# Kernel optimization log

Measured on AMD Instinct MI355X. Metric: run time of the kernel, lower is better.

Reference implementation:

```python
import jax, jax.numpy as jnp
import numpy as np
from jax import lax

B, T, D_IN, D_OUT = 8, 4096, 256, 256


def setup_inputs() -> dict:
    key = jax.random.key(0)
    k1, k2, k3, k4, k5 = jax.random.split(key, 5)
    bound_in = 1.0 / np.sqrt(D_IN)
    return {
        "inputs": jax.random.normal(k1, (B, T, D_IN), dtype=jnp.float32),
        "mask": jnp.zeros((B, T, 1), dtype=jnp.float32),
        "W_in": jax.random.uniform(k2, (D_OUT, D_IN), jnp.float32, -bound_in, bound_in),
        "b_in": jax.random.uniform(k3, (D_OUT,), jnp.float32, -bound_in, bound_in),
        "W_f": jax.random.uniform(k4, (D_OUT, D_IN), jnp.float32, -bound_in, bound_in),
        "b_f": jax.random.uniform(k5, (D_OUT,), jnp.float32, -bound_in, bound_in),
    }


def _forget_mult(f, x):
    # h_t = f_t * x_t + (1 - f_t) * h_{t-1}, h_{-1} = 0 (torchqrnn ForgetMult, hidden_init=None)
    fT = jnp.swapaxes(f, 0, 1)  # (T, B, D)
    xT = jnp.swapaxes(x, 0, 1)

    def step(h, fx):
        ft, xt = fx
        h = ft * xt + (1.0 - ft) * h
        return h, h

    h0 = jnp.zeros(xT.shape[1:], dtype=x.dtype)  # (B, D)
    _, hs = lax.scan(step, h0, (fT, xT))
    return jnp.swapaxes(hs, 0, 1)  # (B, T, D)


def reference(inputs, mask, W_in, b_in, W_f, b_f):
    # right_to_left = False -> no flips
    x = jnp.tanh(jnp.einsum("btd,od->bto", inputs, W_in) + b_in)
    f = jax.nn.sigmoid(jnp.einsum("btd,od->bto", inputs, W_f) + b_f + mask * 10000.0)
    return _forget_mult(f, x)
```

## Files before the change

### kernel.cpp

```cpp
#include <hip/hip_runtime.h>
#include <math.h>


typedef _Float16 f16x8 __attribute__((ext_vector_type(8)));
typedef _Float16 f16x4_t __attribute__((ext_vector_type(4)));
typedef float f32x4 __attribute__((ext_vector_type(4)));

constexpr int B_ = 8, T_ = 4096, D_ = 256, K_ = 256;
constexpr int M_ = B_ * T_;
constexpr int CHUNK = 64;
constexpr int NCH = T_ / CHUNK;

struct alignas(4) XF { _Float16 x, f; };

__device__ __forceinline__ float fexp2(float a) { return __builtin_amdgcn_exp2f(a); }
__device__ __forceinline__ float frcp(float a) { return __builtin_amdgcn_rcpf(a); }
constexpr float L2E = 1.4426950408889634f;

__device__ __forceinline__ float fast_sigmoid(float z) {
  return frcp(1.f + fexp2(-z * L2E));
}
__device__ __forceinline__ float fast_tanh(float z) {
  const float t = fexp2(-2.f * L2E * fabsf(z));
  const float r = (1.f - t) * frcp(1.f + t);
  return copysignf(r, z);
}

__global__ __launch_bounds__(256) void wconv(const float* __restrict__ Win,
                                             const float* __restrict__ Wf,
                                             _Float16* __restrict__ Wh) {
  int i = (blockIdx.x * 256 + threadIdx.x) * 4;
  const float* src = (i < 65536) ? (Win + i) : (Wf + (i - 65536));
  f32x4 v = *(const f32x4*)src;
  f16x4_t o = { (_Float16)v[0], (_Float16)v[1], (_Float16)v[2], (_Float16)v[3] };
  *(f16x4_t*)(Wh + i) = o;
}

__global__ __launch_bounds__(256, 2) void gemm_act(
    const float* __restrict__ A, const _Float16* __restrict__ W,
    const float* __restrict__ bin, const float* __restrict__ bfv,
    const float* __restrict__ mask, XF* __restrict__ xf) {
  const int tid = threadIdx.x;
  const int w = tid >> 6, lane = tid & 63;
  const int quad = lane >> 4, l16 = lane & 15;
  const int mwb = (w >> 1) * 32, nwb = (w & 1) * 128;
  const int row0 = blockIdx.x * 64 + mwb;

  f32x4 acc[2][2][8];
#pragma unroll
  for (int a = 0; a < 2; ++a)
#pragma unroll
    for (int i = 0; i < 2; ++i)
#pragma unroll
      for (int j = 0; j < 8; ++j) acc[a][i][j] = (f32x4){0.f, 0.f, 0.f, 0.f};

  for (int kk = 0; kk < 8; ++kk) {
    const int k0 = kk * 32 + quad * 8;
    f16x8 afr[2];
#pragma unroll
    for (int mt = 0; mt < 2; ++mt) {
      const float* p = A + (size_t)(row0 + mt * 16 + l16) * K_ + k0;
      f32x4 lo = *(const f32x4*)p;
      f32x4 hi = *(const f32x4*)(p + 4);
      f16x8 t;
      t[0] = (_Float16)lo[0]; t[1] = (_Float16)lo[1];
      t[2] = (_Float16)lo[2]; t[3] = (_Float16)lo[3];
      t[4] = (_Float16)hi[0]; t[5] = (_Float16)hi[1];
      t[6] = (_Float16)hi[2]; t[7] = (_Float16)hi[3];
      afr[mt] = t;
    }
#pragma unroll
    for (int mat = 0; mat < 2; ++mat) {
      const _Float16* Wp = W + ((size_t)mat << 16);
      f16x8 bfr[8];
#pragma unroll
      for (int nt = 0; nt < 8; ++nt)
        bfr[nt] = *(const f16x8*)(Wp + (size_t)(nwb + nt * 16 + l16) * K_ + k0);
#pragma unroll
      for (int mt = 0; mt < 2; ++mt)
#pragma unroll
        for (int nt = 0; nt < 8; ++nt)
          acc[mat][mt][nt] = __builtin_amdgcn_mfma_f32_16x16x32_f16(
              afr[mt], bfr[nt], acc[mat][mt][nt], 0, 0, 0);
    }
  }

  float bx[8], bff[8];
#pragma unroll
  for (int nt = 0; nt < 8; ++nt) {
    const int col = nwb + nt * 16 + l16;
    bx[nt] = bin[col];
    bff[nt] = bfv[col];
  }
#pragma unroll
  for (int mt = 0; mt < 2; ++mt) {
#pragma unroll
    for (int r = 0; r < 4; ++r) {
      const int row = row0 + mt * 16 + quad * 4 + r;
      const float madd = 10000.f * mask[row];
#pragma unroll
      for (int nt = 0; nt < 8; ++nt) {
        const int col = nwb + nt * 16 + l16;
        const float zx = acc[0][mt][nt][r] + bx[nt];
        const float zf = acc[1][mt][nt][r] + bff[nt] + madd;
        XF v;
        v.x = (_Float16)fast_tanh(zx);
        v.f = (_Float16)fast_sigmoid(zf);
        xf[(size_t)row * D_ + col] = v;
      }
    }
  }
}

__global__ __launch_bounds__(256) void scan_a(const XF* __restrict__ xf,
                                              float* __restrict__ Ap,
                                              float* __restrict__ Hp) {
  const int d = threadIdx.x;
  const int g = blockIdx.x;
  const size_t base = (size_t)g * CHUNK * D_ + d;
  float Aacc = 1.f, h = 0.f;
#pragma unroll 8
  for (int i = 0; i < CHUNK; ++i) {
    const XF v = xf[base + (size_t)i * D_];
    const float f = (float)v.f;
    const float a = 1.f - f;
    h = f * (float)v.x + a * h;
    Aacc *= a;
  }
  Ap[(size_t)g * D_ + d] = Aacc;
  Hp[(size_t)g * D_ + d] = h;
}

__global__ __launch_bounds__(256) void scan_b(const float* __restrict__ Ap,
                                              const float* __restrict__ Hp,
                                              float* __restrict__ hs) {
  const int d = threadIdx.x, b = blockIdx.x;
  float h = 0.f;
#pragma unroll 8
  for (int c = 0; c < NCH; ++c) {
    const size_t idx = ((size_t)b * NCH + c) * D_ + d;
    hs[idx] = h;
    h = Hp[idx] + Ap[idx] * h;
  }
}

__global__ __launch_bounds__(256) void scan_c(const XF* __restrict__ xf,
                                              const float* __restrict__ hs,
                                              float* __restrict__ out) {
  const int d = threadIdx.x;
  const int g = blockIdx.x;
  float h = hs[(size_t)g * D_ + d];
  const size_t base = (size_t)g * CHUNK * D_ + d;
#pragma unroll 8
  for (int i = 0; i < CHUNK; ++i) {
    const XF v = xf[base + (size_t)i * D_];
    const float f = (float)v.f;
    h = f * (float)v.x + (1.f - f) * h;
    out[base + (size_t)i * D_] = h;
  }
}

extern "C" void kernel_launch(void* const* d_in, const int* in_sizes, int n_in,
                              void* d_out, int out_size, void* d_ws, size_t ws_size,
                              hipStream_t stream) {
  const float* inputs = (const float*)d_in[0];
  const float* mask   = (const float*)d_in[1];
  const float* W_in   = (const float*)d_in[2];
  const float* b_in   = (const float*)d_in[3];
  const float* W_f    = (const float*)d_in[4];
  const float* b_f    = (const float*)d_in[5];
  float* out = (float*)d_out;
  char* ws = (char*)d_ws;

  constexpr size_t XFSZ = (size_t)M_ * D_ * sizeof(XF);
  constexpr size_t WSZ  = (size_t)2 * 256 * 256 * 2;
  constexpr size_t SUM  = (size_t)B_ * NCH * D_ * sizeof(float);

  XF* xf = (XF*)ws;
  _Float16* Wh = (_Float16*)(ws + XFSZ);
  float* Ap = (float*)(ws + XFSZ + WSZ);
  float* Hp = Ap + SUM / sizeof(float);
  float* Hs = Hp + SUM / sizeof(float);

  wconv<<<128, 256, 0, stream>>>(W_in, W_f, Wh);
  gemm_act<<<512, 256, 0, stream>>>(inputs, Wh, b_in, b_f, mask, xf);
  scan_a<<<512, 256, 0, stream>>>(xf, Ap, Hp);
  scan_b<<<8, 256, 0, stream>>>(Ap, Hp, Hs);
  scan_c<<<512, 256, 0, stream>>>(xf, Hs, out);
}
```

Baseline: 151.6 us.

## Fuse chunk scan into LDS-staged GEMM and merge carry propagation into final scan

The GEMM now stages A and a pre-swizzled fp16 weight layout through LDS and uses 32x32x16 MFMA tiles. It writes the activated x/f tile to shared memory and runs the per-chunk scan in the same kernel, which drops the separate scan_a pass that re-read xf. scan_b is removed, and each final-scan block instead recomputes its own carry serially over the preceding chunk summaries. This cuts two launches and one full read of xf. The cost is 64KB of LDS per block, which limits occupancy, and a redundant carry loop of up to 63 steps per block.

```diff
diff --git a/kernel.cpp b/kernel.cpp
--- a/kernel.cpp
+++ b/kernel.cpp
@@ -3,8 +3,8 @@
 
 
 typedef _Float16 f16x8 __attribute__((ext_vector_type(8)));
-typedef _Float16 f16x4_t __attribute__((ext_vector_type(4)));
 typedef float f32x4 __attribute__((ext_vector_type(4)));
+typedef float f32x16 __attribute__((ext_vector_type(16)));
 
 constexpr int B_ = 8, T_ = 4096, D_ = 256, K_ = 256;
 constexpr int M_ = B_ * T_;
@@ -22,44 +22,57 @@
 }
 __device__ __forceinline__ float fast_tanh(float z) {
   const float t = fexp2(-2.f * L2E * fabsf(z));
-  const float r = (1.f - t) * frcp(1.f + t);
-  return copysignf(r, z);
+  return copysignf((1.f - t) * frcp(1.f + t), z);
 }
 
 __global__ __launch_bounds__(256) void wconv(const float* __restrict__ Win,
                                              const float* __restrict__ Wf,
-                                             _Float16* __restrict__ Wh) {
-  int i = (blockIdx.x * 256 + threadIdx.x) * 4;
-  const float* src = (i < 65536) ? (Win + i) : (Wf + (i - 65536));
-  f32x4 v = *(const f32x4*)src;
-  f16x4_t o = { (_Float16)v[0], (_Float16)v[1], (_Float16)v[2], (_Float16)v[3] };
-  *(f16x4_t*)(Wh + i) = o;
-}
-
-__global__ __launch_bounds__(256, 2) void gemm_act(
-    const float* __restrict__ A, const _Float16* __restrict__ W,
+                                             _Float16* __restrict__ Wh2) {
+  const int t = blockIdx.x * 256 + threadIdx.x;
+  const int n = t & 255;
+  const int kc = (t >> 8) & 3;
+  const int mat = (t >> 10) & 1;
+  const int kk = t >> 11;
+  const float* s = (mat ? Wf : Win) + (size_t)n * K_ + kk * 32 + kc * 8;
+  f32x4 a = *(const f32x4*)s;
+  f32x4 b = *(const f32x4*)(s + 4);
+  f16x8 o;
+  o[0] = (_Float16)a[0]; o[1] = (_Float16)a[1];
+  o[2] = (_Float16)a[2]; o[3] = (_Float16)a[3];
+  o[4] = (_Float16)b[0]; o[5] = (_Float16)b[1];
+  o[6] = (_Float16)b[2]; o[7] = (_Float16)b[3];
+  *(f16x8*)(Wh2 + (size_t)t * 8) = o;
+}
+
+__global__ __launch_bounds__(256) void gemm_fused(
+    const float* __restrict__ A, const _Float16* __restrict__ Wh2,
     const float* __restrict__ bin, const float* __restrict__ bfv,
-    const float* __restrict__ mask, XF* __restrict__ xf) {
+    const float* __restrict__ mask, XF* __restrict__ xf,
+    float* __restrict__ Ap, float* __restrict__ Hp) {
+  __shared__ __align__(16) char smem[65536];
+  char* ldsA = smem;
+  char* ldsW = smem + 4096;
+
   const int tid = threadIdx.x;
   const int w = tid >> 6, lane = tid & 63;
-  const int quad = lane >> 4, l16 = lane & 15;
-  const int mwb = (w >> 1) * 32, nwb = (w & 1) * 128;
-  const int row0 = blockIdx.x * 64 + mwb;
-
-  f32x4 acc[2][2][8];
-#pragma unroll
-  for (int a = 0; a < 2; ++a)
-#pragma unroll
-    for (int i = 0; i < 2; ++i)
-#pragma unroll
-      for (int j = 0; j < 8; ++j) acc[a][i][j] = (f32x4){0.f, 0.f, 0.f, 0.f};
+  const int mw = w >> 1, nw = w & 1;
+  const int nl = lane & 31, kh = lane >> 5;
+  const int ml = mw * 32 + nl;
+  const int row0b = blockIdx.x * 64;
+
+  f32x16 acc[2][4];
+#pragma unroll
+  for (int mat = 0; mat < 2; ++mat)
+#pragma unroll
+    for (int nt = 0; nt < 4; ++nt) acc[mat][nt] = (f32x16)(0.f);
+
+  const int am = tid >> 2, apc = tid & 3, akc = (apc - am) & 3;
+  const float* agp = A + (size_t)(row0b + am) * K_ + akc * 8;
+  char* const alds = ldsA + tid * 16;
 
   for (int kk = 0; kk < 8; ++kk) {
-    const int k0 = kk * 32 + quad * 8;
-    f16x8 afr[2];
-#pragma unroll
-    for (int mt = 0; mt < 2; ++mt) {
-      const float* p = A + (size_t)(row0 + mt * 16 + l16) * K_ + k0;
+    {
+      const float* p = agp + kk * 32;
       f32x4 lo = *(const f32x4*)p;
       f32x4 hi = *(const f32x4*)(p + 4);
       f16x8 t;
@@ -67,96 +80,103 @@
       t[2] = (_Float16)lo[2]; t[3] = (_Float16)lo[3];
       t[4] = (_Float16)hi[0]; t[5] = (_Float16)hi[1];
       t[6] = (_Float16)hi[2]; t[7] = (_Float16)hi[3];
-      afr[mt] = t;
-    }
-#pragma unroll
-    for (int mat = 0; mat < 2; ++mat) {
-      const _Float16* Wp = W + ((size_t)mat << 16);
-      f16x8 bfr[8];
-#pragma unroll
-      for (int nt = 0; nt < 8; ++nt)
-        bfr[nt] = *(const f16x8*)(Wp + (size_t)(nwb + nt * 16 + l16) * K_ + k0);
-#pragma unroll
-      for (int mt = 0; mt < 2; ++mt)
-#pragma unroll
-        for (int nt = 0; nt < 8; ++nt)
-          acc[mat][mt][nt] = __builtin_amdgcn_mfma_f32_16x16x32_f16(
-              afr[mt], bfr[nt], acc[mat][mt][nt], 0, 0, 0);
-    }
-  }
-
-  float bx[8], bff[8];
-#pragma unroll
-  for (int nt = 0; nt < 8; ++nt) {
-    const int col = nwb + nt * 16 + l16;
+      *(f16x8*)alds = t;
+    }
+#pragma unroll
+    for (int j = 0; j < 8; ++j) {
+      const int c = j * 256 + tid;
+      f16x8 v = *(const f16x8*)(Wh2 + (size_t)kk * 16384 + (size_t)c * 8);
+      *(f16x8*)(ldsW + (size_t)c * 16) = v;
+    }
+    __syncthreads();
+
+    f16x8 afr[2];
+#pragma unroll
+    for (int i2 = 0; i2 < 2; ++i2) {
+      const int kc = i2 * 2 + kh;
+      const int pc = (kc + ml) & 3;
+      afr[i2] = *(const f16x8*)(ldsA + (ml * 4 + pc) * 16);
+    }
+#pragma unroll
+    for (int mat = 0; mat < 2; ++mat)
+#pragma unroll
+      for (int nt = 0; nt < 4; ++nt) {
+        const int n = nw * 128 + nt * 32 + nl;
+#pragma unroll
+        for (int i2 = 0; i2 < 2; ++i2) {
+          const int kc = i2 * 2 + kh;
+          f16x8 bfr = *(const f16x8*)(ldsW + ((mat * 4 + kc) * 256 + n) * 16);
+          acc[mat][nt] = __builtin_amdgcn_mfma_f32_32x32x16_f16(
+              afr[i2], bfr, acc[mat][nt], 0, 0, 0);
+        }
+      }
+    __syncthreads();
+  }
+
+  float bx[4], bf[4];
+#pragma unroll
+  for (int nt = 0; nt < 4; ++nt) {
+    const int col = nw * 128 + nt * 32 + nl;
     bx[nt] = bin[col];
-    bff[nt] = bfv[col];
-  }
-#pragma unroll
-  for (int mt = 0; mt < 2; ++mt) {
-#pragma unroll
-    for (int r = 0; r < 4; ++r) {
-      const int row = row0 + mt * 16 + quad * 4 + r;
-      const float madd = 10000.f * mask[row];
-#pragma unroll
-      for (int nt = 0; nt < 8; ++nt) {
-        const int col = nwb + nt * 16 + l16;
-        const float zx = acc[0][mt][nt][r] + bx[nt];
-        const float zf = acc[1][mt][nt][r] + bff[nt] + madd;
-        XF v;
-        v.x = (_Float16)fast_tanh(zx);
-        v.f = (_Float16)fast_sigmoid(zf);
-        xf[(size_t)row * D_ + col] = v;
-      }
-    }
-  }
-}
-
-__global__ __launch_bounds__(256) void scan_a(const XF* __restrict__ xf,
-                                              float* __restrict__ Ap,
-                                              float* __restrict__ Hp) {
-  const int d = threadIdx.x;
-  const int g = blockIdx.x;
-  const size_t base = (size_t)g * CHUNK * D_ + d;
-  float Aacc = 1.f, h = 0.f;
+    bf[nt] = bfv[col];
+  }
+  float madd[16];
+  int rowl[16];
+#pragma unroll
+  for (int reg = 0; reg < 16; ++reg) {
+    const int rl = mw * 32 + (reg & 3) + 8 * (reg >> 2) + 4 * kh;
+    rowl[reg] = rl;
+    madd[reg] = 10000.f * mask[row0b + rl];
+  }
+#pragma unroll
+  for (int nt = 0; nt < 4; ++nt) {
+    const int col = nw * 128 + nt * 32 + nl;
+#pragma unroll
+    for (int reg = 0; reg < 16; ++reg) {
+      const float zx = acc[0][nt][reg] + bx[nt];
+      const float zf = acc[1][nt][reg] + bf[nt] + madd[reg];
+      XF v;
+      v.x = (_Float16)fast_tanh(zx);
+      v.f = (_Float16)fast_sigmoid(zf);
+      *(XF*)(smem + ((size_t)rowl[reg] * D_ + col) * 4) = v;
+      xf[((size_t)row0b + rowl[reg]) * D_ + col] = v;
+    }
+  }
+  __syncthreads();
+
+  const int d = tid;
+  float Aa = 1.f, h = 0.f;
 #pragma unroll 8
-  for (int i = 0; i < CHUNK; ++i) {
-    const XF v = xf[base + (size_t)i * D_];
+  for (int t = 0; t < CHUNK; ++t) {
+    const XF v = *(const XF*)(smem + ((size_t)t * D_ + d) * 4);
     const float f = (float)v.f;
     const float a = 1.f - f;
     h = f * (float)v.x + a * h;
-    Aacc *= a;
-  }
-  Ap[(size_t)g * D_ + d] = Aacc;
-  Hp[(size_t)g * D_ + d] = h;
-}
-
-__global__ __launch_bounds__(256) void scan_b(const float* __restrict__ Ap,
-                                              const float* __restrict__ Hp,
-                                              float* __restrict__ hs) {
-  const int d = threadIdx.x, b = blockIdx.x;
+    Aa *= a;
+  }
+  Ap[(size_t)blockIdx.x * D_ + d] = Aa;
+  Hp[(size_t)blockIdx.x * D_ + d] = h;
+}
+
+__global__ __launch_bounds__(256) void scan_final(const XF* __restrict__ xf,
+                                                  const float* __restrict__ Ap,
+                                                  const float* __restrict__ Hp,
+                                                  float* __restrict__ out) {
+  const int g = blockIdx.x;
+  const int b = g >> 6, c = g & 63;
+  const int d = threadIdx.x;
+  const float* ap = Ap + ((size_t)b * NCH) * D_ + d;
+  const float* hp = Hp + ((size_t)b * NCH) * D_ + d;
   float h = 0.f;
-#pragma unroll 8
-  for (int c = 0; c < NCH; ++c) {
-    const size_t idx = ((size_t)b * NCH + c) * D_ + d;
-    hs[idx] = h;
-    h = Hp[idx] + Ap[idx] * h;
-  }
-}
-
-__global__ __launch_bounds__(256) void scan_c(const XF* __restrict__ xf,
-                                              const float* __restrict__ hs,
-                                              float* __restrict__ out) {
-  const int d = threadIdx.x;
-  const int g = blockIdx.x;
-  float h = hs[(size_t)g * D_ + d];
+  for (int j = 0; j < c; ++j) h = hp[(size_t)j * D_] + ap[(size_t)j * D_] * h;
+
   const size_t base = (size_t)g * CHUNK * D_ + d;
 #pragma unroll 8
-  for (int i = 0; i < CHUNK; ++i) {
-    const XF v = xf[base + (size_t)i * D_];
+  for (int t = 0; t < CHUNK; ++t) {
+    const XF v = xf[base + (size_t)t * D_];
     const float f = (float)v.f;
     h = f * (float)v.x + (1.f - f) * h;
-    out[base + (size_t)i * D_] = h;
+    out[base + (size_t)t * D_] = h;
   }
 }
 
@@ -177,14 +197,11 @@
   constexpr size_t SUM  = (size_t)B_ * NCH * D_ * sizeof(float);
 
   XF* xf = (XF*)ws;
-  _Float16* Wh = (_Float16*)(ws + XFSZ);
+  _Float16* Wh2 = (_Float16*)(ws + XFSZ);
   float* Ap = (float*)(ws + XFSZ + WSZ);
   float* Hp = Ap + SUM / sizeof(float);
-  float* Hs = Hp + SUM / sizeof(float);
-
-  wconv<<<128, 256, 0, stream>>>(W_in, W_f, Wh);
-  gemm_act<<<512, 256, 0, stream>>>(inputs, Wh, b_in, b_f, mask, xf);
-  scan_a<<<512, 256, 0, stream>>>(xf, Ap, Hp);
-  scan_b<<<8, 256, 0, stream>>>(Ap, Hp, Hs);
-  scan_c<<<512, 256, 0, stream>>>(xf, Hs, out);
-}
+
+  wconv<<<64, 256, 0, stream>>>(W_in, W_f, Wh2);
+  gemm_fused<<<512, 256, 0, stream>>>(inputs, Wh2, b_in, b_f, mask, xf, Ap, Hp);
+  scan_final<<<512, 256, 0, stream>>>(xf, Ap, Hp, out);
+}
```

After: 141.3 us. 6.8% less time.
